# Kernel optimization log

Measured on AMD Instinct MI355X. Metric: run time of the kernel, lower is better.

The kernel has to match this reference:

```python
import jax, jax.numpy as jnp
import numpy as np

EPS = 1e-8
N_BOXES = 500000


def _make_boxes(key, n):
    k1, k2, k3 = jax.random.split(key, 3)
    center = jax.random.uniform(k1, (n, 3), minval=-40.0, maxval=40.0)
    dims = jax.random.uniform(k2, (n, 3), minval=1.0, maxval=4.0)
    yaw = jax.random.uniform(k3, (n, 1), minval=-np.pi, maxval=np.pi)
    return jnp.concatenate([center, dims, yaw], axis=1).astype(jnp.float32)


def setup_inputs() -> dict:
    key = jax.random.key(0)
    kt, kc, kd, ky = jax.random.split(key, 4)
    target = _make_boxes(kt, N_BOXES)
    # pred = target + small perturbation so IoU is non-trivial
    dc = 0.3 * jax.random.normal(kc, (N_BOXES, 3))
    dd = jnp.exp(0.1 * jax.random.normal(kd, (N_BOXES, 3)))
    dy = 0.1 * jax.random.normal(ky, (N_BOXES, 1))
    pred = jnp.concatenate([target[:, :3] + dc,
                            target[:, 3:6] * dd,
                            target[:, 6:7] + dy], axis=1).astype(jnp.float32)
    weight = jnp.ones((N_BOXES,), dtype=jnp.float32)
    return {"pred": pred, "target": target, "weight": weight}


def box2corners(box):
    # box: (N,5) = (x, y, w, l, alpha) -> BEV corners (N,4,2)
    x, y, w, l, a = (box[:, i] for i in range(5))
    dx = jnp.array([0.5, -0.5, -0.5, 0.5], dtype=box.dtype)
    dy = jnp.array([0.5, 0.5, -0.5, -0.5], dtype=box.dtype)
    xs = dx[None, :] * w[:, None]
    ys = dy[None, :] * l[:, None]
    cos, sin = jnp.cos(a)[:, None], jnp.sin(a)[:, None]
    cx = x[:, None] + xs * cos - ys * sin
    cy = y[:, None] + xs * sin + ys * cos
    return jnp.stack([cx, cy], axis=-1)


def _cross2(a, b):
    return a[..., 0] * b[..., 1] - a[..., 1] * b[..., 0]


def box_intersection(c1, c2):
    # all 4x4 edge-pair intersections between two convex quads
    p1, p2 = c1, jnp.roll(c1, -1, axis=1)          # edges of box1
    q1, q2 = c2, jnp.roll(c2, -1, axis=1)          # edges of box2
    d1 = (p2 - p1)[:, :, None, :]                   # (N,4,1,2)
    d2 = (q2 - q1)[:, None, :, :]                   # (N,1,4,2)
    r = q1[:, None, :, :] - p1[:, :, None, :]       # (N,4,4,2)
    denom = _cross2(d1, d2)                         # (N,4,4)
    safe = jnp.where(jnp.abs(denom) < EPS, 1.0, denom)
    t = _cross2(r, d2) / safe
    u = _cross2(r, d1) / safe
    mask = (jnp.abs(denom) >= EPS) & (t > 0) & (t < 1) & (u > 0) & (u < 1)
    pts = p1[:, :, None, :] + t[..., None] * d1     # (N,4,4,2)
    pts = jnp.where(mask[..., None], pts, 0.0)
    n = c1.shape[0]
    return pts.reshape(n, 16, 2), mask.reshape(n, 16)


def points_in_box(pts, corners):
    # pts (N,4,2) inside rotated rect given by corners (N,4,2)
    a, b, d = corners[:, 0:1], corners[:, 1:2], corners[:, 3:4]
    ab, ad = b - a, d - a
    ap = pts - a
    pab = jnp.sum(ap * ab, -1) / jnp.sum(ab * ab, -1)
    pad = jnp.sum(ap * ad, -1) / jnp.sum(ad * ad, -1)
    e = 1e-6
    return (pab > -e) & (pab < 1 + e) & (pad > -e) & (pad < 1 + e)


def oriented_box_intersection_area(c1, c2):
    inter_pts, inter_mask = box_intersection(c1, c2)
    m1 = points_in_box(c1, c2)
    m2 = points_in_box(c2, c1)
    verts = jnp.concatenate([c1, c2, inter_pts], axis=1)   # (N,24,2)
    mask = jnp.concatenate([m1, m2, inter_mask], axis=1)   # (N,24)
    num = jnp.sum(mask, axis=1, keepdims=True)             # (N,1)
    mean = jnp.sum(verts * mask[..., None], axis=1, keepdims=True) / jnp.maximum(num, 1)[..., None]
    centered = verts - mean
    ang = jnp.arctan2(centered[..., 1], centered[..., 0])
    ang = jnp.where(mask, ang, 1e8)                        # invalid verts sort last
    idx = jnp.argsort(ang, axis=1)
    sv = jnp.take_along_axis(centered, idx[..., None], axis=1)
    sm = jnp.take_along_axis(mask, idx, axis=1)
    first = sv[:, 0:1, :]
    sv = jnp.where(sm[..., None], sv, first)               # pad with first valid vertex
    nxt = jnp.roll(sv, -1, axis=1)
    area = 0.5 * jnp.abs(jnp.sum(_cross2(sv, nxt), axis=1))
    return jnp.where(num[:, 0] > 2, area, 0.0)


def diff_iou_rotated_3d(box1, box2):
    # boxes: (N,7) = (x, y, z, w, l, h, alpha)
    c1 = box2corners(box1[:, jnp.array([0, 1, 3, 4, 6])])
    c2 = box2corners(box2[:, jnp.array([0, 1, 3, 4, 6])])
    inter_area = oriented_box_intersection_area(c1, c2)
    zmax = jnp.minimum(box1[:, 2] + 0.5 * box1[:, 5], box2[:, 2] + 0.5 * box2[:, 5])
    zmin = jnp.maximum(box1[:, 2] - 0.5 * box1[:, 5], box2[:, 2] - 0.5 * box2[:, 5])
    inter_vol = inter_area * jnp.clip(zmax - zmin, 0.0)
    v1 = box1[:, 3] * box1[:, 4] * box1[:, 5]
    v2 = box2[:, 3] * box2[:, 4] * box2[:, 5]
    return inter_vol / (v1 + v2 - inter_vol + EPS)


LOSS_WEIGHT = 1.0


def reference(pred, target, weight):
    iou = diff_iou_rotated_3d(pred, target)
    loss = (1.0 - iou) * weight
    return LOSS_WEIGHT * jnp.mean(loss)  # reduction='mean'
```

## Files before the change

kernel.cpp:

```cpp
#include <hip/hip_runtime.h>
#include <math.h>

#define NTH 256

__device__ __forceinline__ float frcp(float x) { return __builtin_amdgcn_rcpf(x); }

__device__ __forceinline__ float clip_cross(
    float ax, float ay, float bx, float by,
    float ocx, float ocy, float c, float s,
    float heu, float hev)
{
    float dx = bx - ax, dy = by - ay;
    float rx = ax - ocx, ry = ay - ocy;
    float s0u = rx*c + ry*s,  sdu = dx*c + dy*s;
    float s0v = ry*c - rx*s,  sdv = dy*c - dx*s;
    float iu = frcp(sdu), iv = frcp(sdv);
    float ta = (-heu - s0u)*iu, tb = (heu - s0u)*iu;
    float tc = (-hev - s0v)*iv, td = (hev - s0v)*iv;
    float tlu = fminf(ta, tb), thu = fmaxf(ta, tb);
    float tlv = fminf(tc, td), thv = fmaxf(tc, td);
    float tin  = fmaxf(fmaxf(tlu, tlv), 0.0f);
    float tout = fminf(fminf(thu, thv), 1.0f);
    bool ok = tin < tout;
    float Ax = ax + tin*dx,  Ay = ay + tin*dy;
    float Bx = ax + tout*dx, By = ay + tout*dy;
    float cr = Ax*By - Ay*Bx;
    return ok ? cr : 0.0f;
}

__device__ __forceinline__ float iou_loss_one(const float b1[7], const float b2[7], float w)
{
    float zmax = fminf(b1[2]+0.5f*b1[5], b2[2]+0.5f*b2[5]);
    float zmin = fmaxf(b1[2]-0.5f*b1[5], b2[2]-0.5f*b2[5]);
    float dz = fmaxf(zmax - zmin, 0.0f);
    float v1 = b1[3]*b1[4]*b1[5];
    float v2 = b2[3]*b2[4]*b2[5];

    float ox = b2[0] - b1[0], oy = b2[1] - b1[1];
    float ca1 = __cosf(b1[6]), sa1 = __sinf(b1[6]);
    float ca2 = __cosf(b2[6]), sa2 = __sinf(b2[6]);
    float hw1 = 0.5f*b1[3], hl1 = 0.5f*b1[4];
    float hw2 = 0.5f*b2[3], hl2 = 0.5f*b2[4];

    const float dxs[4] = {0.5f,-0.5f,-0.5f,0.5f};
    const float dys[4] = {0.5f,0.5f,-0.5f,-0.5f};
    float px[4], py[4], qx[4], qy[4];
    #pragma unroll
    for (int k = 0; k < 4; ++k) {
        float xs = dxs[k]*b1[3], ys = dys[k]*b1[4];
        px[k] = xs*ca1 - ys*sa1;
        py[k] = xs*sa1 + ys*ca1;
        float xs2 = dxs[k]*b2[3], ys2 = dys[k]*b2[4];
        qx[k] = ox + xs2*ca2 - ys2*sa2;
        qy[k] = oy + xs2*sa2 + ys2*ca2;
    }

    float s2 = 0.0f;
    #pragma unroll
    for (int k = 0; k < 4; ++k) {
        int kn = (k+1)&3;
        s2 += clip_cross(px[k],py[k], px[kn],py[kn], ox,oy, ca2,sa2, hw2,hl2);
        s2 += clip_cross(qx[k],qy[k], qx[kn],qy[kn], 0.0f,0.0f, ca1,sa1, hw1,hl1);
    }
    float area = 0.5f*fabsf(s2);

    float inter_vol = area * dz;
    float iou = inter_vol * frcp(v1 + v2 - inter_vol + 1e-8f);
    return (1.0f - iou) * w;
}

__global__ __launch_bounds__(NTH) void iou_loss_kernel(
    const float* __restrict__ pred, const float* __restrict__ target,
    const float* __restrict__ weight, float* __restrict__ partial, int n)
{
    int i = blockIdx.x * blockDim.x + threadIdx.x;
    float loss = 0.0f;
    if (i < n) {
        float b1[7], b2[7];
        #pragma unroll
        for (int j = 0; j < 7; ++j) { b1[j] = pred[i*7+j]; b2[j] = target[i*7+j]; }
        loss = iou_loss_one(b1, b2, weight[i]);
    }

    #pragma unroll
    for (int off = 32; off > 0; off >>= 1) loss += __shfl_down(loss, off, 64);
    __shared__ float wsum[NTH/64];
    int lane = threadIdx.x & 63, wid = threadIdx.x >> 6;
    if (lane == 0) wsum[wid] = loss;
    __syncthreads();
    if (threadIdx.x == 0) {
        float s = 0.0f;
        #pragma unroll
        for (int w = 0; w < NTH/64; ++w) s += wsum[w];
        partial[blockIdx.x] = s;
    }
}

__global__ __launch_bounds__(NTH) void reduce_kernel(
    const float* __restrict__ partial, int nb, float* __restrict__ out, double inv_n)
{
    double s = 0.0;
    for (int j = threadIdx.x; j < nb; j += NTH) s += (double)partial[j];
    #pragma unroll
    for (int off = 32; off > 0; off >>= 1) s += __shfl_down(s, off, 64);
    __shared__ double wsum[NTH/64];
    int lane = threadIdx.x & 63, wid = threadIdx.x >> 6;
    if (lane == 0) wsum[wid] = s;
    __syncthreads();
    if (threadIdx.x == 0) {
        double tot = 0.0;
        #pragma unroll
        for (int w = 0; w < NTH/64; ++w) tot += wsum[w];
        out[0] = (float)(tot * inv_n);
    }
}

extern "C" void kernel_launch(void* const* d_in, const int* in_sizes, int n_in,
                              void* d_out, int out_size, void* d_ws, size_t ws_size,
                              hipStream_t stream) {
    const float* pred   = (const float*)d_in[0];
    const float* target = (const float*)d_in[1];
    const float* weight = (const float*)d_in[2];
    int n = in_sizes[2];
    float* partial = (float*)d_ws;
    int nblocks = (n + NTH - 1) / NTH;
    hipLaunchKernelGGL(iou_loss_kernel, dim3(nblocks), dim3(NTH), 0, stream,
                       pred, target, weight, partial, n);
    hipLaunchKernelGGL(reduce_kernel, dim3(1), dim3(NTH), 0, stream,
                       partial, nblocks, (float*)d_out, 1.0 / (double)n);
}
```

Measured before the change: 15.68 us.

## Compute box clipping in box1's local frame with relative-rotation algebra

The polygon-clipping area is now computed in the coordinate frame of box1, so box1's edges are axis-aligned and box2 is expressed through the relative angle. Clipping box2's edges against box1 needs no projection, and the cross-product contribution of box1's edges reduces to a sum of clipped parameter lengths times a constant. Reciprocals are shared across edges. This cuts ALU work per box pair at the cost of an extra sin/cos pair and more complex code whose numerical edge cases, such as axis-parallel edges giving infinite reciprocals, need care.

```diff
diff --git a/kernel.cpp b/kernel.cpp
--- a/kernel.cpp
+++ b/kernel.cpp
@@ -4,29 +4,6 @@
 #define NTH 256
 
 __device__ __forceinline__ float frcp(float x) { return __builtin_amdgcn_rcpf(x); }
-
-__device__ __forceinline__ float clip_cross(
-    float ax, float ay, float bx, float by,
-    float ocx, float ocy, float c, float s,
-    float heu, float hev)
-{
-    float dx = bx - ax, dy = by - ay;
-    float rx = ax - ocx, ry = ay - ocy;
-    float s0u = rx*c + ry*s,  sdu = dx*c + dy*s;
-    float s0v = ry*c - rx*s,  sdv = dy*c - dx*s;
-    float iu = frcp(sdu), iv = frcp(sdv);
-    float ta = (-heu - s0u)*iu, tb = (heu - s0u)*iu;
-    float tc = (-hev - s0v)*iv, td = (hev - s0v)*iv;
-    float tlu = fminf(ta, tb), thu = fmaxf(ta, tb);
-    float tlv = fminf(tc, td), thv = fmaxf(tc, td);
-    float tin  = fmaxf(fmaxf(tlu, tlv), 0.0f);
-    float tout = fminf(fminf(thu, thv), 1.0f);
-    bool ok = tin < tout;
-    float Ax = ax + tin*dx,  Ay = ay + tin*dy;
-    float Bx = ax + tout*dx, By = ay + tout*dy;
-    float cr = Ax*By - Ay*Bx;
-    return ok ? cr : 0.0f;
-}
 
 __device__ __forceinline__ float iou_loss_one(const float b1[7], const float b2[7], float w)
 {
@@ -36,34 +13,82 @@
     float v1 = b1[3]*b1[4]*b1[5];
     float v2 = b2[3]*b2[4]*b2[5];
 
-    float ox = b2[0] - b1[0], oy = b2[1] - b1[1];
-    float ca1 = __cosf(b1[6]), sa1 = __sinf(b1[6]);
-    float ca2 = __cosf(b2[6]), sa2 = __sinf(b2[6]);
     float hw1 = 0.5f*b1[3], hl1 = 0.5f*b1[4];
     float hw2 = 0.5f*b2[3], hl2 = 0.5f*b2[4];
 
-    const float dxs[4] = {0.5f,-0.5f,-0.5f,0.5f};
-    const float dys[4] = {0.5f,0.5f,-0.5f,-0.5f};
-    float px[4], py[4], qx[4], qy[4];
-    #pragma unroll
-    for (int k = 0; k < 4; ++k) {
-        float xs = dxs[k]*b1[3], ys = dys[k]*b1[4];
-        px[k] = xs*ca1 - ys*sa1;
-        py[k] = xs*sa1 + ys*ca1;
-        float xs2 = dxs[k]*b2[3], ys2 = dys[k]*b2[4];
-        qx[k] = ox + xs2*ca2 - ys2*sa2;
-        qy[k] = oy + xs2*sa2 + ys2*ca2;
-    }
+    float da = b2[6] - b1[6];
+    float ct = __cosf(da), st = __sinf(da);
+    float ca1 = __cosf(b1[6]), sa1 = __sinf(b1[6]);
+    float ox = b2[0] - b1[0], oy = b2[1] - b1[1];
+    float Ox =  ox*ca1 + oy*sa1;
+    float Oy =  oy*ca1 - ox*sa1;
+
+    float ux = hw2*ct, uy = hw2*st;
+    float vx = -hl2*st, vy = hl2*ct;
+
+    float wx_ = ux+vx, wy_ = uy+vy, zx_ = ux-vx, zy_ = uy-vy;
+    float q0x = Ox+wx_, q0y = Oy+wy_;
+    float q1x = Ox-zx_, q1y = Oy-zy_;
+    float q2x = Ox-wx_, q2y = Oy-wy_;
+    float q3x = Ox+zx_, q3y = Oy+zy_;
+
+    float i2ux = frcp(ux+ux), i2uy = frcp(uy+uy);
+    float i2vx = frcp(vx+vx), i2vy = frcp(vy+vy);
 
     float s2 = 0.0f;
-    #pragma unroll
-    for (int k = 0; k < 4; ++k) {
-        int kn = (k+1)&3;
-        s2 += clip_cross(px[k],py[k], px[kn],py[kn], ox,oy, ca2,sa2, hw2,hl2);
-        s2 += clip_cross(qx[k],qy[k], qx[kn],qy[kn], 0.0f,0.0f, ca1,sa1, hw1,hl1);
-    }
+
+    #define CLIP_Q(AX,AY,DX,DY,IUX,IUY)  {                                  \
+        float ta = (-hw1 - (AX))*(IUX), tb = (hw1 - (AX))*(IUX);            \
+        float tc = (-hl1 - (AY))*(IUY), td = (hl1 - (AY))*(IUY);            \
+        float tlu = fminf(ta,tb), thu = fmaxf(ta,tb);                       \
+        float tlv = fminf(tc,td), thv = fmaxf(tc,td);                       \
+        float tin  = fmaxf(fmaxf(tlu,tlv), 0.0f);                           \
+        float tout = fminf(fminf(thu,thv), 1.0f);                           \
+        bool ok = tin < tout;                                               \
+        float Apx = (AX) + tin*(DX),  Apy = (AY) + tin*(DY);                \
+        float Bpx = (AX) + tout*(DX), Bpy = (AY) + tout*(DY);               \
+        float cr = Apx*Bpy - Apy*Bpx;                                       \
+        s2 += ok ? cr : 0.0f; }
+
+    CLIP_Q(q0x,q0y, -(ux+ux), -(uy+uy), -i2ux, -i2uy)
+    CLIP_Q(q1x,q1y, -(vx+vx), -(vy+vy), -i2vx, -i2vy)
+    CLIP_Q(q2x,q2y,  (ux+ux),  (uy+uy),  i2ux,  i2uy)
+    CLIP_Q(q3x,q3y,  (vx+vx),  (vy+vy),  i2vx,  i2vy)
+    #undef CLIP_Q
+
+    #define PROJ(PX,PY,PU,PV) { float rx=(PX)-Ox, ry=(PY)-Oy;               \
+        PU = rx*ct + ry*st;  PV = ry*ct - rx*st; }
+    float p0u,p0v,p1u,p1v,p2u,p2v,p3u,p3v;
+    PROJ( hw1,  hl1, p0u,p0v)
+    PROJ(-hw1,  hl1, p1u,p1v)
+    PROJ(-hw1, -hl1, p2u,p2v)
+    PROJ( hw1, -hl1, p3u,p3v)
+    #undef PROJ
+
+    float Au = (hw1+hw1)*ct, Av = (hw1+hw1)*st;
+    float Cu = (hl1+hl1)*st, Cv = (hl1+hl1)*ct;
+    float iAu = frcp(Au), iAv = frcp(Av), iCu = frcp(Cu), iCv = frcp(Cv);
+
+    float sdt = 0.0f;
+    #define CLIP_P(PU,PV,IDU,IDV) {                                         \
+        float ta = (-hw2 - (PU))*(IDU), tb = (hw2 - (PU))*(IDU);            \
+        float tc = (-hl2 - (PV))*(IDV), td = (hl2 - (PV))*(IDV);            \
+        float tlu = fminf(ta,tb), thu = fmaxf(ta,tb);                       \
+        float tlv = fminf(tc,td), thv = fmaxf(tc,td);                       \
+        float tin  = fmaxf(fmaxf(tlu,tlv), 0.0f);                           \
+        float tout = fminf(fminf(thu,thv), 1.0f);                           \
+        float dt = tout - tin;                                              \
+        sdt += (dt > 0.0f) ? dt : 0.0f; }
+
+    CLIP_P(p0u,p0v, -iAu,  iAv)
+    CLIP_P(p1u,p1v, -iCu, -iCv)
+    CLIP_P(p2u,p2v,  iAu, -iAv)
+    CLIP_P(p3u,p3v,  iCu,  iCv)
+    #undef CLIP_P
+
+    s2 += (hw1+hw1)*hl1*sdt;
+
     float area = 0.5f*fabsf(s2);
-
     float inter_vol = area * dz;
     float iou = inter_vol * frcp(v1 + v2 - inter_vol + 1e-8f);
     return (1.0f - iou) * w;
```

New measurement: 13.42 us. -14.4%, faster.
